# Kernel tuning notes

Measured on AMD Instinct MI355X. Metric: run time of the kernel, lower is better.

Reference implementation:

```python
import jax, jax.numpy as jnp
import numpy as np

B, D_IN, H = 16384, 512, 1024


def setup_inputs() -> dict:
    key = jax.random.key(0)
    ks = jax.random.split(key, 12)
    s_in = 1.0 / np.sqrt(D_IN)
    s_h = 1.0 / np.sqrt(H)
    d = {
        "input_x": jax.random.normal(ks[0], (B, D_IN), jnp.float32),
        "h_old": jax.random.normal(ks[1], (B, H), jnp.float32),
        "c_old": jax.random.normal(ks[2], (B, H), jnp.float32),
    }
    names_U = ["Ui", "Uf", "Uo", "Uc"]
    names_W = ["Wi", "Wf", "Wo", "Wc"]
    for i, n in enumerate(names_U):
        d[n + "_w"] = jax.random.normal(ks[3 + i], (D_IN, H), jnp.float32) * s_in
        d[n + "_b"] = jnp.zeros((H,), jnp.float32)
    for i, n in enumerate(names_W):
        d[n + "_w"] = jax.random.normal(ks[7 + i], (H, H), jnp.float32) * s_h
        d[n + "_b"] = jnp.zeros((H,), jnp.float32)
    return d


def reference(input_x, h_old, c_old,
              Ui_w, Ui_b, Wi_w, Wi_b,
              Uf_w, Uf_b, Wf_w, Wf_b,
              Uo_w, Uo_b, Wo_w, Wo_b,
              Uc_w, Uc_b, Wc_w, Wc_b):
    # Fuse the 8 small GEMMs into 2: concatenate gate projections along the
    # output dim (math identical to 8 separate Dense layers + adds).
    U = jnp.concatenate([Ui_w, Uf_w, Uo_w, Uc_w], axis=1)   # [D_in, 4H]
    W = jnp.concatenate([Wi_w, Wf_w, Wo_w, Wc_w], axis=1)   # [H, 4H]
    b = jnp.concatenate([Ui_b + Wi_b, Uf_b + Wf_b, Uo_b + Wo_b, Uc_b + Wc_b])
    gates = input_x @ U + h_old @ W + b                      # [B, 4H]
    i_t, f_t, o_t, g_t = jnp.split(gates, 4, axis=1)
    i_t = jax.nn.sigmoid(i_t)
    f_t = jax.nn.sigmoid(f_t)
    o_t = jax.nn.sigmoid(o_t)
    c_t = jnp.tanh(g_t)
    c = i_t * c_t + f_t * c_old
    h_new = o_t * jnp.tanh(c)
    return (h_new, c)
```

## Files before the change

### kernel.cpp

```cpp
#include <hip/hip_runtime.h>
#include <hip/hip_bf16.h>
#include <stdint.h>

#define B_ROWS 16384
#define D_IN   512
#define H_DIM  1024
#define K_TOT  1536
#define NKT    48
#define NIT    12

typedef __attribute__((ext_vector_type(8)))  short bf16x8;
typedef __attribute__((ext_vector_type(16))) float f32x16;
typedef __attribute__((ext_vector_type(4)))  float float4v;
typedef __attribute__((ext_vector_type(8)))  unsigned short u16x8;

__device__ __forceinline__ unsigned short f2bf(float f) {
    uint32_t u = __float_as_uint(f);
    u = (u + 0x7FFFu + ((u >> 16) & 1u)) >> 16;
    return (unsigned short)u;
}

__global__ void cvt_A(const float* __restrict__ x, const float* __restrict__ h,
                      unsigned short* __restrict__ Ag) {
    int t     = blockIdx.x * blockDim.x + threadIdx.x;
    int lane  = t & 63;
    int chunk = (t >> 6) & 15;
    int rest  = t >> 10;
    int tile  = rest % 48;
    int bm    = rest / 48;
    int row   = bm * 256 + (chunk >> 1) * 32 + (lane & 31);
    int k     = tile * 32 + (chunk & 1) * 16 + (lane >> 5) * 8;
    const float* src = (k < 512) ? (x + (size_t)row * D_IN + k)
                                 : (h + (size_t)row * H_DIM + (k - 512));
    float4v v0 = *(const float4v*)(src);
    float4v v1 = *(const float4v*)(src + 4);
    u16x8 o;
    o[0] = f2bf(v0[0]); o[1] = f2bf(v0[1]); o[2] = f2bf(v0[2]); o[3] = f2bf(v0[3]);
    o[4] = f2bf(v1[0]); o[5] = f2bf(v1[1]); o[6] = f2bf(v1[2]); o[7] = f2bf(v1[3]);
    *(u16x8*)(Ag + (size_t)t * 8) = o;
}

__global__ void cvt_B(const float* __restrict__ Ui, const float* __restrict__ Uf,
                      const float* __restrict__ Uo, const float* __restrict__ Uc,
                      const float* __restrict__ Wi, const float* __restrict__ Wf,
                      const float* __restrict__ Wo, const float* __restrict__ Wc,
                      unsigned short* __restrict__ Bg) {
    int t     = blockIdx.x * blockDim.x + threadIdx.x;
    int lane  = t & 63;
    int chunk = (t >> 6) & 15;
    int rest  = t >> 10;
    int tile  = rest % 48;
    int bn    = rest / 48;
    int c     = bn * 256 + (chunk >> 1) * 32 + (lane & 31);
    int g     = (c >> 5) & 3;
    int hcol  = ((c >> 7) << 5) | (c & 31);
    int k     = tile * 32 + (chunk & 1) * 16 + (lane >> 5) * 8;
    const float* up = (g == 0) ? Ui : (g == 1) ? Uf : (g == 2) ? Uo : Uc;
    const float* wp = (g == 0) ? Wi : (g == 1) ? Wf : (g == 2) ? Wo : Wc;
    u16x8 o;
    if (k < 512) {
        const float* s = up + (size_t)k * H_DIM + hcol;
        #pragma unroll
        for (int i = 0; i < 8; ++i) o[i] = f2bf(s[(size_t)i * H_DIM]);
    } else {
        const float* s = wp + (size_t)(k - 512) * H_DIM + hcol;
        #pragma unroll
        for (int i = 0; i < 8; ++i) o[i] = f2bf(s[(size_t)i * H_DIM]);
    }
    *(u16x8*)(Bg + (size_t)t * 8) = o;
}

__global__ void cvt_bias(const float* __restrict__ Uib, const float* __restrict__ Ufb,
                         const float* __restrict__ Uob, const float* __restrict__ Ucb,
                         const float* __restrict__ Wib, const float* __restrict__ Wfb,
                         const float* __restrict__ Wob, const float* __restrict__ Wcb,
                         float* __restrict__ bias) {
    int t = blockIdx.x * blockDim.x + threadIdx.x;
    int g = t >> 10, h = t & 1023;
    const float* ub = (g == 0) ? Uib : (g == 1) ? Ufb : (g == 2) ? Uob : Ucb;
    const float* wb = (g == 0) ? Wib : (g == 1) ? Wfb : (g == 2) ? Wob : Wcb;
    bias[t] = ub[h] + wb[h];
}

__global__ __launch_bounds__(512, 2) void lstm_gemm(
        const unsigned short* __restrict__ Ag, const unsigned short* __restrict__ Bg,
        const float* __restrict__ bias, const float* __restrict__ c_old,
        float* __restrict__ out) {
    __shared__ __align__(1024) char lds[131072];

    const int tid = threadIdx.x;
    const int l   = tid & 63;
    const int wv  = tid >> 6;
    const int wm  = wv >> 1;
    const int wn  = wv & 1;

    const int orig = blockIdx.x;
    const int xcd  = orig & 7;
    const int jj   = orig >> 3;
    const int bn   = (xcd & 3) * 4 + (jj & 3);
    const int bm   = (xcd >> 2) * 32 + (jj >> 2);

    const unsigned short* aT = Ag + (size_t)(wv * 2) * 512 + l * 8;
    const unsigned short* bT = Bg + (size_t)(wv * 2) * 512 + l * 8;
    const size_t aTileBase = (size_t)bm * 48 * 8192;
    const size_t bTileBase = (size_t)bn * 48 * 8192;

#define GLDS(SRC, DST) __builtin_amdgcn_global_load_lds(                            \
        (const __attribute__((address_space(1))) void*)(SRC),                       \
        (__attribute__((address_space(3))) void*)(DST), 16, 0, 0)

#define STAGE(ST, SLOT) do {                                                        \
    const unsigned short* _a = aT + aTileBase + (size_t)(ST) * 8192;                \
    const unsigned short* _b = bT + bTileBase + (size_t)(ST) * 8192;                \
    char* _da = (char*)lds + (SLOT) * 32768 + (wv * 2) * 1024;                      \
    char* _db = _da + 16384;                                                        \
    GLDS(_a,       _da);        GLDS(_a + 512, _da + 1024);                         \
    GLDS(_b,       _db);        GLDS(_b + 512, _db + 1024);                         \
} while (0)

    f32x16 acc[2][4] = {};

#define PHASE(P, ST) do {                                                           \
    const char* _Ab = (const char*)lds + (P) * 32768 + wm * 4096 + l * 16;          \
    const char* _Bb = (const char*)lds + (P) * 32768 + 16384 + wn * 8192 + l * 16;  \
    bf16x8 aF[2][2], bF[4][2];                                                      \
    _Pragma("unroll") for (int mm = 0; mm < 2; ++mm)                                \
        _Pragma("unroll") for (int ks = 0; ks < 2; ++ks)                            \
            aF[mm][ks] = *(const bf16x8*)(_Ab + mm * 2048 + ks * 1024);             \
    _Pragma("unroll") for (int nn = 0; nn < 4; ++nn)                                \
        _Pragma("unroll") for (int ks = 0; ks < 2; ++ks)                            \
            bF[nn][ks] = *(const bf16x8*)(_Bb + nn * 2048 + ks * 1024);             \
    STAGE(ST, ((P) + 3) & 3);                                                       \
    __builtin_amdgcn_s_setprio(1);                                                  \
    _Pragma("unroll") for (int ks = 0; ks < 2; ++ks)                                \
        _Pragma("unroll") for (int mm = 0; mm < 2; ++mm)                            \
            _Pragma("unroll") for (int nn = 0; nn < 4; ++nn)                        \
                acc[mm][nn] = __builtin_amdgcn_mfma_f32_32x32x16_bf16(              \
                    aF[mm][ks], bF[nn][ks], acc[mm][nn], 0, 0, 0);                  \
    __builtin_amdgcn_s_setprio(0);                                                  \
    asm volatile("s_waitcnt vmcnt(8)\ns_barrier" ::: "memory");                     \
} while (0)

    STAGE(0, 0); STAGE(1, 1); STAGE(2, 2);
    asm volatile("s_waitcnt vmcnt(8)\ns_barrier" ::: "memory");

    #pragma unroll 1
    for (int i = 0; i < NIT; ++i) {
        const int b4 = i * 4;
        int s0 = b4 + 3;
        int s1 = b4 + 4; if (s1 >= NKT) s1 -= NKT;
        int s2 = b4 + 5; if (s2 >= NKT) s2 -= NKT;
        int s3 = b4 + 6; if (s3 >= NKT) s3 -= NKT;
        PHASE(0, s0);
        PHASE(1, s1);
        PHASE(2, s2);
        PHASE(3, s3);
    }
    asm volatile("s_waitcnt vmcnt(0)" ::: "memory");

    const int r31 = l & 31;
    const int h5  = l >> 5;
    const int hh  = (bn * 2 + wn) * 32 + r31;
    const float bi  = bias[hh];
    const float bff = bias[1024 + hh];
    const float bo  = bias[2048 + hh];
    const float bc  = bias[3072 + hh];

    #pragma unroll
    for (int mm = 0; mm < 2; ++mm) {
        const int rb = bm * 256 + wm * 64 + mm * 32 + 4 * h5;
        #pragma unroll
        for (int r = 0; r < 16; ++r) {
            const int row = rb + (r & 3) + 8 * (r >> 2);
            float iv = acc[mm][0][r] + bi;
            float fv = acc[mm][1][r] + bff;
            float ov = acc[mm][2][r] + bo;
            float gv = acc[mm][3][r] + bc;
            float it = 1.f / (1.f + __expf(-iv));
            float ft = 1.f / (1.f + __expf(-fv));
            float ot = 1.f / (1.f + __expf(-ov));
            float gt = 1.f - 2.f / (1.f + __expf(2.f * gv));
            float co = c_old[(size_t)row * H_DIM + hh];
            float cn = it * gt + ft * co;
            float th = 1.f - 2.f / (1.f + __expf(2.f * cn));
            out[(size_t)row * H_DIM + hh] = ot * th;
            out[(size_t)B_ROWS * H_DIM + (size_t)row * H_DIM + hh] = cn;
        }
    }
#undef PHASE
#undef STAGE
#undef GLDS
}

extern "C" void kernel_launch(void* const* d_in, const int* in_sizes, int n_in,
                              void* d_out, int out_size, void* d_ws, size_t ws_size,
                              hipStream_t stream) {
    const float* x  = (const float*)d_in[0];
    const float* h0 = (const float*)d_in[1];
    const float* c0 = (const float*)d_in[2];
    const float* Uw[4] = {(const float*)d_in[3],  (const float*)d_in[5],
                          (const float*)d_in[7],  (const float*)d_in[9]};
    const float* Ub[4] = {(const float*)d_in[4],  (const float*)d_in[6],
                          (const float*)d_in[8],  (const float*)d_in[10]};
    const float* Ww[4] = {(const float*)d_in[11], (const float*)d_in[13],
                          (const float*)d_in[15], (const float*)d_in[17]};
    const float* Wb[4] = {(const float*)d_in[12], (const float*)d_in[14],
                          (const float*)d_in[16], (const float*)d_in[18]};

    unsigned short* Ag = (unsigned short*)d_ws;
    unsigned short* Bg = Ag + (size_t)B_ROWS * K_TOT;
    float* bias        = (float*)(Bg + (size_t)4096 * K_TOT);
    float* out         = (float*)d_out;

    cvt_A<<<12288, 256, 0, stream>>>(x, h0, Ag);
    cvt_B<<<3072, 256, 0, stream>>>(Uw[0], Uw[1], Uw[2], Uw[3],
                                    Ww[0], Ww[1], Ww[2], Ww[3], Bg);
    cvt_bias<<<16, 256, 0, stream>>>(Ub[0], Ub[1], Ub[2], Ub[3],
                                     Wb[0], Wb[1], Wb[2], Wb[3], bias);
    lstm_gemm<<<1024, 512, 0, stream>>>(Ag, Bg, bias, c0, out);
}
```

Baseline: 274.1 us.

## Deepen LDS pipeline to five stages with split barriers and alternate vmcnt gating

The GEMM main loop moves from a 4-slot to a 5-slot LDS ring buffer (160KB), prefetching four k-tiles ahead instead of three. Each phase now issues a barrier and an lgkmcnt wait after the fragment reads and before the MFMAs. The vmcnt wait is applied only on every other phase, so loads have more time to land and global latency is better hidden. In exchange the kernel uses more LDS (likely cutting occupancy to one block per CU), adds an extra barrier per phase, and issues redundant dummy loads in the tail.

```diff
diff --git a/kernel.cpp b/kernel.cpp
--- a/kernel.cpp
+++ b/kernel.cpp
@@ -7,7 +7,6 @@
 #define H_DIM  1024
 #define K_TOT  1536
 #define NKT    48
-#define NIT    12
 
 typedef __attribute__((ext_vector_type(8)))  short bf16x8;
 typedef __attribute__((ext_vector_type(16))) float f32x16;
@@ -86,7 +85,7 @@
         const unsigned short* __restrict__ Ag, const unsigned short* __restrict__ Bg,
         const float* __restrict__ bias, const float* __restrict__ c_old,
         float* __restrict__ out) {
-    __shared__ __align__(1024) char lds[131072];
+    __shared__ __align__(1024) char lds[163840];
 
     const int tid = threadIdx.x;
     const int l   = tid & 63;
@@ -120,9 +119,9 @@
 
     f32x16 acc[2][4] = {};
 
-#define PHASE(P, ST) do {                                                           \
-    const char* _Ab = (const char*)lds + (P) * 32768 + wm * 4096 + l * 16;          \
-    const char* _Bb = (const char*)lds + (P) * 32768 + 16384 + wn * 8192 + l * 16;  \
+#define PHASE(SLOT, ST, SSLOT, GATE) do {                                           \
+    const char* _Ab = (const char*)lds + (SLOT) * 32768 + wm * 4096 + l * 16;       \
+    const char* _Bb = (const char*)lds + (SLOT) * 32768 + 16384 + wn * 8192 + l * 16;\
     bf16x8 aF[2][2], bF[4][2];                                                      \
     _Pragma("unroll") for (int mm = 0; mm < 2; ++mm)                                \
         _Pragma("unroll") for (int ks = 0; ks < 2; ++ks)                            \
@@ -130,7 +129,10 @@
     _Pragma("unroll") for (int nn = 0; nn < 4; ++nn)                                \
         _Pragma("unroll") for (int ks = 0; ks < 2; ++ks)                            \
             bF[nn][ks] = *(const bf16x8*)(_Bb + nn * 2048 + ks * 1024);             \
-    STAGE(ST, ((P) + 3) & 3);                                                       \
+    STAGE(ST, SSLOT);                                                               \
+    asm volatile("s_barrier" ::: "memory");                                         \
+    asm volatile("s_waitcnt lgkmcnt(0)" ::: "memory");                              \
+    __builtin_amdgcn_sched_barrier(0);                                              \
     __builtin_amdgcn_s_setprio(1);                                                  \
     _Pragma("unroll") for (int ks = 0; ks < 2; ++ks)                                \
         _Pragma("unroll") for (int mm = 0; mm < 2; ++mm)                            \
@@ -138,24 +140,37 @@
                 acc[mm][nn] = __builtin_amdgcn_mfma_f32_32x32x16_bf16(              \
                     aF[mm][ks], bF[nn][ks], acc[mm][nn], 0, 0, 0);                  \
     __builtin_amdgcn_s_setprio(0);                                                  \
-    asm volatile("s_waitcnt vmcnt(8)\ns_barrier" ::: "memory");                     \
+    if (GATE) { asm volatile("s_waitcnt vmcnt(8)\ns_barrier" ::: "memory"); }       \
+    else      { asm volatile("s_barrier" ::: "memory"); }                           \
 } while (0)
 
-    STAGE(0, 0); STAGE(1, 1); STAGE(2, 2);
+    STAGE(0, 0); STAGE(1, 1); STAGE(2, 2); STAGE(3, 3);
     asm volatile("s_waitcnt vmcnt(8)\ns_barrier" ::: "memory");
 
     #pragma unroll 1
-    for (int i = 0; i < NIT; ++i) {
-        const int b4 = i * 4;
-        int s0 = b4 + 3;
-        int s1 = b4 + 4; if (s1 >= NKT) s1 -= NKT;
-        int s2 = b4 + 5; if (s2 >= NKT) s2 -= NKT;
-        int s3 = b4 + 6; if (s3 >= NKT) s3 -= NKT;
-        PHASE(0, s0);
-        PHASE(1, s1);
-        PHASE(2, s2);
-        PHASE(3, s3);
+    for (int i = 0; i < 4; ++i) {
+        const int T = i * 10;
+        PHASE(0, T + 4,  4, 0);
+        PHASE(1, T + 5,  0, 1);
+        PHASE(2, T + 6,  1, 0);
+        PHASE(3, T + 7,  2, 1);
+        PHASE(4, T + 8,  3, 0);
+        PHASE(0, T + 9,  4, 1);
+        PHASE(1, T + 10, 0, 0);
+        PHASE(2, T + 11, 1, 1);
+        PHASE(3, T + 12, 2, 0);
+        PHASE(4, T + 13, 3, 1);
     }
+
+    PHASE(0, 44, 4, 0);
+    PHASE(1, 45, 0, 1);
+    PHASE(2, 46, 1, 0);
+    PHASE(3, 47, 2, 1);
+    PHASE(4, 0,  3, 0);
+    PHASE(0, 0,  4, 1);
+    PHASE(1, 0,  0, 0);
+    PHASE(2, 0,  1, 1);
+
     asm volatile("s_waitcnt vmcnt(0)" ::: "memory");
 
     const int r31 = l & 31;
```

Measured after the change: 272.2 us. Within noise of the previous version (-0.7%).

## Deepen LDS pipeline to five stages and double-buffer register fragments

Applied to the files above, without the earlier changes.

Grows shared memory from four to five 32KB stages and restructures the main loop so LDS fragment reads for the next k-tile happen before the MFMAs of the current one, using two register fragment buffers. It also removes the wraparound redundant loads of the old schedule by running an explicit drain epilogue. The aim is to hide LDS read latency behind MFMA work and keep more global loads in flight. The cost is 160KB of LDS per block, which likely drops occupancy from the two blocks per CU declared in the launch bounds to one, plus higher register pressure from the doubled fragments.

```diff
diff --git a/kernel.cpp b/kernel.cpp
--- a/kernel.cpp
+++ b/kernel.cpp
@@ -7,7 +7,6 @@
 #define H_DIM  1024
 #define K_TOT  1536
 #define NKT    48
-#define NIT    12
 
 typedef __attribute__((ext_vector_type(8)))  short bf16x8;
 typedef __attribute__((ext_vector_type(16))) float f32x16;
@@ -86,7 +85,7 @@
         const unsigned short* __restrict__ Ag, const unsigned short* __restrict__ Bg,
         const float* __restrict__ bias, const float* __restrict__ c_old,
         float* __restrict__ out) {
-    __shared__ __align__(1024) char lds[131072];
+    __shared__ __align__(1024) char lds[163840];
 
     const int tid = threadIdx.x;
     const int l   = tid & 63;
@@ -100,63 +99,75 @@
     const int bn   = (xcd & 3) * 4 + (jj & 3);
     const int bm   = (xcd >> 2) * 32 + (jj >> 2);
 
-    const unsigned short* aT = Ag + (size_t)(wv * 2) * 512 + l * 8;
-    const unsigned short* bT = Bg + (size_t)(wv * 2) * 512 + l * 8;
-    const size_t aTileBase = (size_t)bm * 48 * 8192;
-    const size_t bTileBase = (size_t)bn * 48 * 8192;
+    const unsigned short* aCur = Ag + (size_t)bm * 48 * 8192 + (size_t)(wv * 2) * 512 + l * 8;
+    const unsigned short* bCur = Bg + (size_t)bn * 48 * 8192 + (size_t)(wv * 2) * 512 + l * 8;
+
+    const int aRdOff = wm * 4096 + l * 16;
+    const int bRdOff = 16384 + wn * 8192 + l * 16;
+
+    int rdOff = 0;
+    int stOff = 0;
 
 #define GLDS(SRC, DST) __builtin_amdgcn_global_load_lds(                            \
         (const __attribute__((address_space(1))) void*)(SRC),                       \
         (__attribute__((address_space(3))) void*)(DST), 16, 0, 0)
 
-#define STAGE(ST, SLOT) do {                                                        \
-    const unsigned short* _a = aT + aTileBase + (size_t)(ST) * 8192;                \
-    const unsigned short* _b = bT + bTileBase + (size_t)(ST) * 8192;                \
-    char* _da = (char*)lds + (SLOT) * 32768 + (wv * 2) * 1024;                      \
-    char* _db = _da + 16384;                                                        \
-    GLDS(_a,       _da);        GLDS(_a + 512, _da + 1024);                         \
-    GLDS(_b,       _db);        GLDS(_b + 512, _db + 1024);                         \
+#define STAGE_T() do {                                                              \
+    char* _d = (char*)lds + stOff + wv * 2048;                                      \
+    GLDS(aCur,       _d);            GLDS(aCur + 512, _d + 1024);                   \
+    GLDS(bCur,       _d + 16384);    GLDS(bCur + 512, _d + 16384 + 1024);           \
+    aCur += 8192; bCur += 8192;                                                     \
+    stOff = (stOff == 131072) ? 0 : stOff + 32768;                                  \
 } while (0)
 
-    f32x16 acc[2][4] = {};
-
-#define PHASE(P, ST) do {                                                           \
-    const char* _Ab = (const char*)lds + (P) * 32768 + wm * 4096 + l * 16;          \
-    const char* _Bb = (const char*)lds + (P) * 32768 + 16384 + wn * 8192 + l * 16;  \
-    bf16x8 aF[2][2], bF[4][2];                                                      \
+#define READS(FR) do {                                                              \
+    const char* _pA = (const char*)lds + rdOff + aRdOff;                            \
+    const char* _pB = (const char*)lds + rdOff + bRdOff;                            \
     _Pragma("unroll") for (int mm = 0; mm < 2; ++mm)                                \
         _Pragma("unroll") for (int ks = 0; ks < 2; ++ks)                            \
-            aF[mm][ks] = *(const bf16x8*)(_Ab + mm * 2048 + ks * 1024);             \
+            FR[mm * 2 + ks] = *(const bf16x8*)(_pA + mm * 2048 + ks * 1024);        \
     _Pragma("unroll") for (int nn = 0; nn < 4; ++nn)                                \
         _Pragma("unroll") for (int ks = 0; ks < 2; ++ks)                            \
-            bF[nn][ks] = *(const bf16x8*)(_Bb + nn * 2048 + ks * 1024);             \
-    STAGE(ST, ((P) + 3) & 3);                                                       \
+            FR[4 + nn * 2 + ks] = *(const bf16x8*)(_pB + nn * 2048 + ks * 1024);    \
+    rdOff = (rdOff == 131072) ? 0 : rdOff + 32768;                                  \
+} while (0)
+
+    f32x16 acc[2][4] = {};
+
+#define MFMAS(FR) do {                                                              \
     __builtin_amdgcn_s_setprio(1);                                                  \
     _Pragma("unroll") for (int ks = 0; ks < 2; ++ks)                                \
         _Pragma("unroll") for (int mm = 0; mm < 2; ++mm)                            \
             _Pragma("unroll") for (int nn = 0; nn < 4; ++nn)                        \
                 acc[mm][nn] = __builtin_amdgcn_mfma_f32_32x32x16_bf16(              \
-                    aF[mm][ks], bF[nn][ks], acc[mm][nn], 0, 0, 0);                  \
+                    FR[mm * 2 + ks], FR[4 + nn * 2 + ks], acc[mm][nn], 0, 0, 0);    \
     __builtin_amdgcn_s_setprio(0);                                                  \
-    asm volatile("s_waitcnt vmcnt(8)\ns_barrier" ::: "memory");                     \
 } while (0)
 
-    STAGE(0, 0); STAGE(1, 1); STAGE(2, 2);
-    asm volatile("s_waitcnt vmcnt(8)\ns_barrier" ::: "memory");
+#define GATE(N) asm volatile("s_waitcnt vmcnt(" #N ")\ns_barrier" ::: "memory")
+
+    bf16x8 fr0[12], fr1[12];
+
+    STAGE_T(); STAGE_T(); STAGE_T(); STAGE_T();
+    GATE(8);
+    READS(fr0);
 
     #pragma unroll 1
-    for (int i = 0; i < NIT; ++i) {
-        const int b4 = i * 4;
-        int s0 = b4 + 3;
-        int s1 = b4 + 4; if (s1 >= NKT) s1 -= NKT;
-        int s2 = b4 + 5; if (s2 >= NKT) s2 -= NKT;
-        int s3 = b4 + 6; if (s3 >= NKT) s3 -= NKT;
-        PHASE(0, s0);
-        PHASE(1, s1);
-        PHASE(2, s2);
-        PHASE(3, s3);
+    for (int i = 0; i < 22; ++i) {
+        READS(fr1);
+        STAGE_T();
+        MFMAS(fr0);
+        GATE(8);
+        READS(fr0);
+        STAGE_T();
+        MFMAS(fr1);
+        GATE(8);
     }
-    asm volatile("s_waitcnt vmcnt(0)" ::: "memory");
+
+    READS(fr1);  MFMAS(fr0);  GATE(4);
+    READS(fr0);  MFMAS(fr1);  GATE(0);
+    READS(fr1);  MFMAS(fr0);  asm volatile("s_barrier" ::: "memory");
+    MFMAS(fr1);
 
     const int r31 = l & 31;
     const int h5  = l >> 5;
@@ -187,8 +198,10 @@
             out[(size_t)B_ROWS * H_DIM + (size_t)row * H_DIM + hh] = cn;
         }
     }
-#undef PHASE
-#undef STAGE
+#undef GATE
+#undef MFMAS
+#undef READS
+#undef STAGE_T
 #undef GLDS
 }
 
```

Measured after the change: 276.0 us. No clear change (+0.7%).

## Load A fragments directly to registers and deepen B LDS pipeline to five stages

Applied to the files above, without the earlier changes.

Each warp now loads its A fragments straight from global memory into registers, double-buffered across phases, so the A tile no longer goes through LDS. LDS holds only B tiles, in a five-slot ring with rotating offsets, which shrinks LDS from 128KB to 80KB and lets B prefetch run further ahead. The waitcnt accounting now mixes register loads with LDS DMA loads. Warps that share wm re-read the same A data from global or L2 instead of sharing it through LDS, and register pressure rises.

```diff
diff --git a/kernel.cpp b/kernel.cpp
--- a/kernel.cpp
+++ b/kernel.cpp
@@ -7,7 +7,6 @@
 #define H_DIM  1024
 #define K_TOT  1536
 #define NKT    48
-#define NIT    12
 
 typedef __attribute__((ext_vector_type(8)))  short bf16x8;
 typedef __attribute__((ext_vector_type(16))) float f32x16;
@@ -86,7 +85,7 @@
         const unsigned short* __restrict__ Ag, const unsigned short* __restrict__ Bg,
         const float* __restrict__ bias, const float* __restrict__ c_old,
         float* __restrict__ out) {
-    __shared__ __align__(1024) char lds[131072];
+    __shared__ __align__(1024) char lds[81920];
 
     const int tid = threadIdx.x;
     const int l   = tid & 63;
@@ -100,61 +99,72 @@
     const int bn   = (xcd & 3) * 4 + (jj & 3);
     const int bm   = (xcd >> 2) * 32 + (jj >> 2);
 
-    const unsigned short* aT = Ag + (size_t)(wv * 2) * 512 + l * 8;
-    const unsigned short* bT = Bg + (size_t)(wv * 2) * 512 + l * 8;
-    const size_t aTileBase = (size_t)bm * 48 * 8192;
-    const size_t bTileBase = (size_t)bn * 48 * 8192;
+    const unsigned short* aBase =
+        Ag + ((size_t)bm * 48 * 16 + 4 * wm) * 512 + l * 8;
+    const unsigned short* bStage =
+        Bg + ((size_t)bn * 48 * 16 + 2 * wv) * 512 + l * 8;
+    const int bRd = wn * 8192 + l * 16;
 
 #define GLDS(SRC, DST) __builtin_amdgcn_global_load_lds(                            \
         (const __attribute__((address_space(1))) void*)(SRC),                       \
         (__attribute__((address_space(3))) void*)(DST), 16, 0, 0)
 
-#define STAGE(ST, SLOT) do {                                                        \
-    const unsigned short* _a = aT + aTileBase + (size_t)(ST) * 8192;                \
-    const unsigned short* _b = bT + bTileBase + (size_t)(ST) * 8192;                \
-    char* _da = (char*)lds + (SLOT) * 32768 + (wv * 2) * 1024;                      \
-    char* _db = _da + 16384;                                                        \
-    GLDS(_a,       _da);        GLDS(_a + 512, _da + 1024);                         \
-    GLDS(_b,       _db);        GLDS(_b + 512, _db + 1024);                         \
+#define STAGE(T, SLOTOFF) do {                                                      \
+    const unsigned short* _s = bStage + (size_t)(T) * 8192;                         \
+    char* _d = (char*)lds + (SLOTOFF) + wv * 2048;                                  \
+    GLDS(_s, _d);  GLDS(_s + 512, _d + 1024);                                       \
 } while (0)
 
+#define ALOAD(AF, T) do {                                                           \
+    const unsigned short* _a = aBase + (size_t)(T) * 8192;                          \
+    AF[0] = *(const u16x8*)(_a);                                                    \
+    AF[1] = *(const u16x8*)(_a + 512);                                              \
+    AF[2] = *(const u16x8*)(_a + 1024);                                             \
+    AF[3] = *(const u16x8*)(_a + 1536);                                             \
+} while (0)
+
     f32x16 acc[2][4] = {};
 
-#define PHASE(P, ST) do {                                                           \
-    const char* _Ab = (const char*)lds + (P) * 32768 + wm * 4096 + l * 16;          \
-    const char* _Bb = (const char*)lds + (P) * 32768 + 16384 + wn * 8192 + l * 16;  \
-    bf16x8 aF[2][2], bF[4][2];                                                      \
-    _Pragma("unroll") for (int mm = 0; mm < 2; ++mm)                                \
-        _Pragma("unroll") for (int ks = 0; ks < 2; ++ks)                            \
-            aF[mm][ks] = *(const bf16x8*)(_Ab + mm * 2048 + ks * 1024);             \
+#define PHASE(RDOFF, AC, AN, TA, TS, STOFF) do {                                    \
+    const char* _B = (const char*)lds + (RDOFF) + bRd;                              \
+    bf16x8 bF[4][2];                                                                \
     _Pragma("unroll") for (int nn = 0; nn < 4; ++nn)                                \
         _Pragma("unroll") for (int ks = 0; ks < 2; ++ks)                            \
-            bF[nn][ks] = *(const bf16x8*)(_Bb + nn * 2048 + ks * 1024);             \
-    STAGE(ST, ((P) + 3) & 3);                                                       \
+            bF[nn][ks] = *(const bf16x8*)(_B + (nn * 2 + ks) * 1024);               \
+    ALOAD(AN, TA);                                                                  \
+    STAGE(TS, STOFF);                                                               \
     __builtin_amdgcn_s_setprio(1);                                                  \
     _Pragma("unroll") for (int ks = 0; ks < 2; ++ks)                                \
         _Pragma("unroll") for (int mm = 0; mm < 2; ++mm)                            \
             _Pragma("unroll") for (int nn = 0; nn < 4; ++nn)                        \
                 acc[mm][nn] = __builtin_amdgcn_mfma_f32_32x32x16_bf16(              \
-                    aF[mm][ks], bF[nn][ks], acc[mm][nn], 0, 0, 0);                  \
+                    (bf16x8)AC[mm * 2 + ks], bF[nn][ks], acc[mm][nn], 0, 0, 0);     \
     __builtin_amdgcn_s_setprio(0);                                                  \
     asm volatile("s_waitcnt vmcnt(8)\ns_barrier" ::: "memory");                     \
 } while (0)
 
-    STAGE(0, 0); STAGE(1, 1); STAGE(2, 2);
+    u16x8 a0[4], a1[4];
+
+    STAGE(0, 0); STAGE(1, 16384); STAGE(2, 32768); STAGE(3, 49152);
+    ALOAD(a0, 0);
     asm volatile("s_waitcnt vmcnt(8)\ns_barrier" ::: "memory");
 
+    int rdOff = 0;
+    int stOff = 65536;
+
     #pragma unroll 1
-    for (int i = 0; i < NIT; ++i) {
-        const int b4 = i * 4;
-        int s0 = b4 + 3;
-        int s1 = b4 + 4; if (s1 >= NKT) s1 -= NKT;
-        int s2 = b4 + 5; if (s2 >= NKT) s2 -= NKT;
-        int s3 = b4 + 6; if (s3 >= NKT) s3 -= NKT;
-        PHASE(0, s0);
-        PHASE(1, s1);
-        PHASE(2, s2);
-        PHASE(3, s3);
+    for (int i = 0; i < 24; ++i) {
+        const int p0 = 2 * i;
+        int tA0 = p0 + 1;
+        int tS0 = p0 + 4;  if (tS0 >= NKT) tS0 -= NKT;
+        PHASE(rdOff, a0, a1, tA0, tS0, stOff);
+        rdOff = (rdOff == 65536) ? 0 : rdOff + 16384;
+        stOff = (stOff == 65536) ? 0 : stOff + 16384;
+        int tA1 = p0 + 2;  if (tA1 >= NKT) tA1 -= NKT;
+        int tS1 = p0 + 5;  if (tS1 >= NKT) tS1 -= NKT;
+        PHASE(rdOff, a1, a0, tA1, tS1, stOff);
+        rdOff = (rdOff == 65536) ? 0 : rdOff + 16384;
+        stOff = (stOff == 65536) ? 0 : stOff + 16384;
     }
     asm volatile("s_waitcnt vmcnt(0)" ::: "memory");
 
@@ -188,6 +198,7 @@
         }
     }
 #undef PHASE
+#undef ALOAD
 #undef STAGE
 #undef GLDS
 }
```

New measurement: 294.6 us. 7.5% more time.
